# Optimization experiments

Hardware: AMD Instinct MI355X
Metric: run time of the kernel (lower is better)

The kernel has to match this reference:

```python
import jax, jax.numpy as jnp
import numpy as np

N_NODES = 10000
N_EDGES = 160000
N_TYPES = 128          # rows in SymbolicEmbeddingsVQ table
N_SYMBOLS = 64
PATTERN_LEN = 8
SYMBOL_DIM = 16
HIDDEN = PATTERN_LEN * SYMBOL_DIM  # mode='concat' -> 128
NUM_RADIAL = 6


def setup_inputs() -> dict:
    key = jax.random.key(0)
    ks = jax.random.split(key, 10)
    x = jax.random.randint(ks[0], (N_NODES,), 0, N_TYPES)
    rbf = jax.random.normal(ks[1], (N_EDGES, NUM_RADIAL), dtype=jnp.float32)
    i = jax.random.randint(ks[2], (N_EDGES,), 0, N_NODES)
    j = jax.random.randint(ks[3], (N_EDGES,), 0, N_NODES)
    # VQ symbolic embedding params: each of 128 types is a pattern of
    # PATTERN_LEN symbol ids; symbols are vectors from a codebook.
    code_idx = jax.random.randint(ks[4], (N_TYPES, PATTERN_LEN), 0, N_SYMBOLS)
    codebook = jax.random.normal(ks[5], (N_SYMBOLS, SYMBOL_DIM), dtype=jnp.float32)
    # Linear layers (PyTorch Linear default uniform init approximated by scaled normals)
    W_rbf = jax.random.normal(ks[6], (NUM_RADIAL, HIDDEN), dtype=jnp.float32) / np.sqrt(NUM_RADIAL)
    b_rbf = jnp.zeros((HIDDEN,), dtype=jnp.float32)
    W = jax.random.normal(ks[7], (3 * HIDDEN, HIDDEN), dtype=jnp.float32) / np.sqrt(3 * HIDDEN)
    b = jnp.zeros((HIDDEN,), dtype=jnp.float32)
    return {"x": x, "rbf": rbf, "i": i, "j": j, "code_idx": code_idx,
            "codebook": codebook, "W_rbf": W_rbf, "b_rbf": b_rbf, "W": W, "b": b}


def reference(x, rbf, i, j, code_idx, codebook, W_rbf, b_rbf, W, b):
    act = jax.nn.silu
    # Symbolic VQ embedding, mode='concat': table[t] = concat of PATTERN_LEN codebook vectors
    table = codebook[code_idx].reshape(N_TYPES, HIDDEN)   # [128, hidden]
    h = table[x]                                          # [N_nodes, hidden]
    r = act(rbf @ W_rbf + b_rbf)                          # [E, hidden]
    feat = jnp.concatenate([h[i], h[j], r], axis=-1)      # [E, 3*hidden]
    return act(feat @ W + b)                              # [E, hidden]
```

## Files before the change

kernel.cpp:

```cpp
#include <hip/hip_runtime.h>
#include <hip/hip_bf16.h>
#include <stdint.h>

typedef __attribute__((ext_vector_type(8))) short bf16x8;
typedef __attribute__((ext_vector_type(4))) float f32x4;

__device__ __forceinline__ float silu_f(float x) {
    return x / (1.0f + __expf(-x));
}

__device__ __forceinline__ unsigned short f2bf(float x) {
    union { float f; unsigned int u; } v; v.f = x;
    unsigned int r = v.u + 0x7fffu + ((v.u >> 16) & 1u);
    return (unsigned short)(r >> 16);
}
__device__ __forceinline__ float bf2f(unsigned short u) {
    union { unsigned int u; float f; } v; v.u = ((unsigned int)u) << 16;
    return v.f;
}

__device__ __forceinline__ void async16(void* l, const void* g) {
    auto lds3 = (__attribute__((address_space(3))) unsigned int*)(uintptr_t)l;
    auto g1   = (const __attribute__((address_space(1))) unsigned int*)(uintptr_t)g;
    __builtin_amdgcn_global_load_lds(g1, lds3, 16, 0, 0);
}

__global__ void prep_P(const int* __restrict__ code_idx,
                       const float* __restrict__ codebook,
                       const float* __restrict__ W,
                       const float* __restrict__ b,
                       unsigned short* __restrict__ P1,
                       unsigned short* __restrict__ P2,
                       unsigned short* __restrict__ Wt3)
{
    __shared__ float trow[128];
    const int t = blockIdx.x, tid = threadIdx.x;
    if (tid < 128) {
        int sym = code_idx[t * 8 + (tid >> 4)];
        trow[tid] = codebook[sym * 16 + (tid & 15)];
    } else {
        int k = tid - 128;
        Wt3[t * 128 + k] = f2bf(W[(256 + k) * 128 + t]);
    }
    __syncthreads();
    const int which = tid >> 7, o = tid & 127;
    const float* Wb = W + which * 16384;
    float acc = which ? 0.0f : b[o];
#pragma unroll 8
    for (int k = 0; k < 128; ++k)
        acc += trow[k] * Wb[k * 128 + o];
    (which ? P2 : P1)[t * 128 + o] = f2bf(acc);
}

__global__ __launch_bounds__(256, 2) void fused_main(
    const int* __restrict__ x,
    const float* __restrict__ rbf,
    const int* __restrict__ ei,
    const int* __restrict__ ej,
    const float* __restrict__ W_rbf,
    const float* __restrict__ b_rbf,
    const unsigned short* __restrict__ P1,
    const unsigned short* __restrict__ P2,
    const unsigned short* __restrict__ Wt3,
    float* __restrict__ out)
{
    __shared__ __align__(16) unsigned char lA[32768];
    __shared__ __align__(16) unsigned char lB[32768];

    const int tid  = threadIdx.x;
    const int lane = tid & 63;
    const int w    = tid >> 6;
    const int e0   = blockIdx.x * 128;

    {
        const int ri = lane >> 4;
        const int ch = lane & 15;
#pragma unroll
        for (int rr = 0; rr < 8; ++rr) {
            int g = w * 8 + rr;
            int o = g * 4 + ri;
            int j = ch ^ (o & 7);
            async16(lB + g * 1024, Wt3 + o * 128 + j * 8);
        }
    }

    {
        const int j16 = tid & 15;
        const int gg  = tid >> 4;
        const int cb  = j16 * 8;
        float wr[6][8];
#pragma unroll
        for (int q = 0; q < 6; ++q) {
            const float4* p = (const float4*)(W_rbf + q * 128 + cb);
            float4 a = p[0], c = p[1];
            wr[q][0]=a.x; wr[q][1]=a.y; wr[q][2]=a.z; wr[q][3]=a.w;
            wr[q][4]=c.x; wr[q][5]=c.y; wr[q][6]=c.z; wr[q][7]=c.w;
        }
        float br[8];
        {
            const float4* p = (const float4*)(b_rbf + cb);
            float4 a = p[0], c = p[1];
            br[0]=a.x; br[1]=a.y; br[2]=a.z; br[3]=a.w;
            br[4]=c.x; br[5]=c.y; br[6]=c.z; br[7]=c.w;
        }
#pragma unroll
        for (int i = 0; i < 8; ++i) {
            int m = gg * 8 + i;
            const float* rr = rbf + (size_t)(e0 + m) * 6;
            float f0=rr[0], f1=rr[1], f2=rr[2], f3=rr[3], f4=rr[4], f5=rr[5];
            bf16x8 pk;
#pragma unroll
            for (int c = 0; c < 8; ++c) {
                float acc = br[c] + f0*wr[0][c] + f1*wr[1][c] + f2*wr[2][c]
                                  + f3*wr[3][c] + f4*wr[4][c] + f5*wr[5][c];
                pk[c] = (short)f2bf(silu_f(acc));
            }
            int p = j16 ^ (m & 7);
            *(bf16x8*)(lA + m * 256 + p * 16) = pk;
        }
    }

    __syncthreads();

    f32x4 acc[4][4] = {};
    const int wm = (w >> 1) * 64, wn = (w & 1) * 64;
    const int quad = lane >> 4, l15 = lane & 15, l7 = lane & 7;
#pragma unroll
    for (int ks = 0; ks < 4; ++ks) {
        const int j = ks * 4 + quad;
        const int p = j ^ l7;
        bf16x8 af[4], bfv[4];
#pragma unroll
        for (int mi = 0; mi < 4; ++mi) {
            int m = wm + mi * 16 + l15;
            af[mi]  = *(const bf16x8*)(lA + m * 256 + p * 16);
            int o = wn + mi * 16 + l15;
            bfv[mi] = *(const bf16x8*)(lB + o * 256 + p * 16);
        }
#pragma unroll
        for (int mi = 0; mi < 4; ++mi)
#pragma unroll
            for (int ni = 0; ni < 4; ++ni)
                acc[mi][ni] = __builtin_amdgcn_mfma_f32_16x16x32_bf16(
                    af[mi], bfv[ni], acc[mi][ni], 0, 0, 0);
    }

#pragma unroll
    for (int mi = 0; mi < 4; ++mi) {
#pragma unroll
        for (int r = 0; r < 4; ++r) {
            int m = wm + mi * 16 + quad * 4 + r;
            int e = e0 + m;
            int ti = x[ei[e]], tj = x[ej[e]];
            const unsigned short* p1r = P1 + ti * 128;
            const unsigned short* p2r = P2 + tj * 128;
#pragma unroll
            for (int ni = 0; ni < 4; ++ni) {
                int o = wn + ni * 16 + l15;
                float v = acc[mi][ni][r] + bf2f(p1r[o]) + bf2f(p2r[o]);
                out[(size_t)e * 128 + o] = silu_f(v);
            }
        }
    }
}

extern "C" void kernel_launch(void* const* d_in, const int* in_sizes, int n_in,
                              void* d_out, int out_size, void* d_ws, size_t ws_size,
                              hipStream_t stream) {
    const int*   x        = (const int*)d_in[0];
    const float* rbf      = (const float*)d_in[1];
    const int*   ei       = (const int*)d_in[2];
    const int*   ej       = (const int*)d_in[3];
    const int*   code_idx = (const int*)d_in[4];
    const float* codebook = (const float*)d_in[5];
    const float* W_rbf    = (const float*)d_in[6];
    const float* b_rbf    = (const float*)d_in[7];
    const float* W        = (const float*)d_in[8];
    const float* b        = (const float*)d_in[9];
    float* out = (float*)d_out;

    const int nE = in_sizes[2];

    if (ws_size < 98304) return;
    unsigned short* P1  = (unsigned short*)d_ws;
    unsigned short* P2  = P1 + 16384;
    unsigned short* Wt3 = P2 + 16384;

    prep_P<<<128, 256, 0, stream>>>(code_idx, codebook, W, b, P1, P2, Wt3);
    fused_main<<<nE / 128, 256, 0, stream>>>(x, rbf, ei, ej, W_rbf, b_rbf,
                                             P1, P2, Wt3, out);
}
```

Baseline: 142.9 us.

## Halve edge tile, stage rbf via async LDS load, prefetch gather indices early

Halves the edges per block from 128 to 64, which shrinks LDS for the A tile and raises the occupancy hint to 3 blocks per SM. The rbf rows are now loaded into LDS with async global-to-LDS copies. The x[ei]/x[ej] index gathers and the P1/P2 row loads are issued before the MFMA loop, so their latency overlaps the rbf compute and the matmul. Silu now uses a hardware reciprocal instead of a division. In exchange, each block reloads the 32KB Wt3 tile for half as many edges, doubling that traffic, and the extra barrier adds sync cost.

```diff
diff --git a/kernel.cpp b/kernel.cpp
--- a/kernel.cpp
+++ b/kernel.cpp
@@ -6,7 +6,7 @@
 typedef __attribute__((ext_vector_type(4))) float f32x4;
 
 __device__ __forceinline__ float silu_f(float x) {
-    return x / (1.0f + __expf(-x));
+    return x * __builtin_amdgcn_rcpf(1.0f + __expf(-x));
 }
 
 __device__ __forceinline__ unsigned short f2bf(float x) {
@@ -52,7 +52,7 @@
     (which ? P2 : P1)[t * 128 + o] = f2bf(acc);
 }
 
-__global__ __launch_bounds__(256, 2) void fused_main(
+__global__ __launch_bounds__(256, 3) void fused_main(
     const int* __restrict__ x,
     const float* __restrict__ rbf,
     const int* __restrict__ ei,
@@ -64,17 +64,20 @@
     const unsigned short* __restrict__ Wt3,
     float* __restrict__ out)
 {
-    __shared__ __align__(16) unsigned char lA[32768];
     __shared__ __align__(16) unsigned char lB[32768];
+    __shared__ __align__(16) unsigned char lA[16384];
+    __shared__ __align__(16) unsigned char lR[1536];
 
     const int tid  = threadIdx.x;
     const int lane = tid & 63;
     const int w    = tid >> 6;
-    const int e0   = blockIdx.x * 128;
+    const int e0   = blockIdx.x * 64;
+
+    const int quad = lane >> 4, l15 = lane & 15;
+    const int wm = (w >> 1) * 32, wn = (w & 1) * 64;
 
     {
-        const int ri = lane >> 4;
-        const int ch = lane & 15;
+        const int ri = lane >> 4, ch = lane & 15;
 #pragma unroll
         for (int rr = 0; rr < 8; ++rr) {
             int g = w * 8 + rr;
@@ -83,62 +86,89 @@
             async16(lB + g * 1024, Wt3 + o * 128 + j * 8);
         }
     }
-
+    if (w == 0)
+        async16(lR, (const unsigned char*)rbf + (size_t)e0 * 24 + lane * 16);
+    else if (w == 1 && lane < 32)
+        async16(lR + 1024, (const unsigned char*)rbf + (size_t)e0 * 24 + 1024 + lane * 16);
+
+    int ti[8], tj[8];
+#pragma unroll
+    for (int mi = 0; mi < 2; ++mi)
+#pragma unroll
+        for (int r = 0; r < 4; ++r) {
+            int m = wm + mi * 16 + quad * 4 + r;
+            int e = e0 + m;
+            ti[mi * 4 + r] = x[ei[e]];
+            tj[mi * 4 + r] = x[ej[e]];
+        }
+
+    const int j16 = tid & 15, gg = tid >> 4, cb = j16 * 8;
+    float wr[6][8], br[8];
+#pragma unroll
+    for (int q = 0; q < 6; ++q) {
+        const float4* p = (const float4*)(W_rbf + q * 128 + cb);
+        float4 a = p[0], c = p[1];
+        wr[q][0]=a.x; wr[q][1]=a.y; wr[q][2]=a.z; wr[q][3]=a.w;
+        wr[q][4]=c.x; wr[q][5]=c.y; wr[q][6]=c.z; wr[q][7]=c.w;
+    }
     {
-        const int j16 = tid & 15;
-        const int gg  = tid >> 4;
-        const int cb  = j16 * 8;
-        float wr[6][8];
-#pragma unroll
-        for (int q = 0; q < 6; ++q) {
-            const float4* p = (const float4*)(W_rbf + q * 128 + cb);
-            float4 a = p[0], c = p[1];
-            wr[q][0]=a.x; wr[q][1]=a.y; wr[q][2]=a.z; wr[q][3]=a.w;
-            wr[q][4]=c.x; wr[q][5]=c.y; wr[q][6]=c.z; wr[q][7]=c.w;
-        }
-        float br[8];
-        {
-            const float4* p = (const float4*)(b_rbf + cb);
-            float4 a = p[0], c = p[1];
-            br[0]=a.x; br[1]=a.y; br[2]=a.z; br[3]=a.w;
-            br[4]=c.x; br[5]=c.y; br[6]=c.z; br[7]=c.w;
-        }
-#pragma unroll
-        for (int i = 0; i < 8; ++i) {
-            int m = gg * 8 + i;
-            const float* rr = rbf + (size_t)(e0 + m) * 6;
-            float f0=rr[0], f1=rr[1], f2=rr[2], f3=rr[3], f4=rr[4], f5=rr[5];
-            bf16x8 pk;
-#pragma unroll
-            for (int c = 0; c < 8; ++c) {
-                float acc = br[c] + f0*wr[0][c] + f1*wr[1][c] + f2*wr[2][c]
-                                  + f3*wr[3][c] + f4*wr[4][c] + f5*wr[5][c];
-                pk[c] = (short)f2bf(silu_f(acc));
+        const float4* p = (const float4*)(b_rbf + cb);
+        float4 a = p[0], c = p[1];
+        br[0]=a.x; br[1]=a.y; br[2]=a.z; br[3]=a.w;
+        br[4]=c.x; br[5]=c.y; br[6]=c.z; br[7]=c.w;
+    }
+
+    __syncthreads();
+
+#pragma unroll
+    for (int i = 0; i < 4; ++i) {
+        int m = gg * 4 + i;
+        const float* rr_ = (const float*)(lR + m * 24);
+        float f0 = rr_[0], f1 = rr_[1], f2 = rr_[2],
+              f3 = rr_[3], f4 = rr_[4], f5 = rr_[5];
+        bf16x8 pk;
+#pragma unroll
+        for (int c = 0; c < 8; ++c) {
+            float a = br[c] + f0*wr[0][c] + f1*wr[1][c] + f2*wr[2][c]
+                            + f3*wr[3][c] + f4*wr[4][c] + f5*wr[5][c];
+            pk[c] = (short)f2bf(silu_f(a));
+        }
+        int p = j16 ^ (m & 7);
+        *(bf16x8*)(lA + m * 256 + p * 16) = pk;
+    }
+
+    __syncthreads();
+
+    unsigned short q1[2][4][4], q2[2][4][4];
+#pragma unroll
+    for (int mi = 0; mi < 2; ++mi)
+#pragma unroll
+        for (int r = 0; r < 4; ++r) {
+            const unsigned short* p1r = P1 + ti[mi * 4 + r] * 128;
+            const unsigned short* p2r = P2 + tj[mi * 4 + r] * 128;
+#pragma unroll
+            for (int ni = 0; ni < 4; ++ni) {
+                int o = wn + ni * 16 + l15;
+                q1[mi][r][ni] = p1r[o];
+                q2[mi][r][ni] = p2r[o];
             }
-            int p = j16 ^ (m & 7);
-            *(bf16x8*)(lA + m * 256 + p * 16) = pk;
-        }
-    }
-
-    __syncthreads();
-
-    f32x4 acc[4][4] = {};
-    const int wm = (w >> 1) * 64, wn = (w & 1) * 64;
-    const int quad = lane >> 4, l15 = lane & 15, l7 = lane & 7;
+        }
+
+    f32x4 acc[2][4] = {};
+    const int l7 = l15 & 7;
 #pragma unroll
     for (int ks = 0; ks < 4; ++ks) {
         const int j = ks * 4 + quad;
         const int p = j ^ l7;
-        bf16x8 af[4], bfv[4];
-#pragma unroll
-        for (int mi = 0; mi < 4; ++mi) {
-            int m = wm + mi * 16 + l15;
-            af[mi]  = *(const bf16x8*)(lA + m * 256 + p * 16);
-            int o = wn + mi * 16 + l15;
-            bfv[mi] = *(const bf16x8*)(lB + o * 256 + p * 16);
-        }
-#pragma unroll
-        for (int mi = 0; mi < 4; ++mi)
+        bf16x8 af[2], bfv[4];
+#pragma unroll
+        for (int mi = 0; mi < 2; ++mi)
+            af[mi] = *(const bf16x8*)(lA + (wm + mi * 16 + l15) * 256 + p * 16);
+#pragma unroll
+        for (int ni = 0; ni < 4; ++ni)
+            bfv[ni] = *(const bf16x8*)(lB + (wn + ni * 16 + l15) * 256 + p * 16);
+#pragma unroll
+        for (int mi = 0; mi < 2; ++mi)
 #pragma unroll
             for (int ni = 0; ni < 4; ++ni)
                 acc[mi][ni] = __builtin_amdgcn_mfma_f32_16x16x32_bf16(
@@ -146,22 +176,18 @@
     }
 
 #pragma unroll
-    for (int mi = 0; mi < 4; ++mi) {
+    for (int mi = 0; mi < 2; ++mi)
 #pragma unroll
         for (int r = 0; r < 4; ++r) {
             int m = wm + mi * 16 + quad * 4 + r;
-            int e = e0 + m;
-            int ti = x[ei[e]], tj = x[ej[e]];
-            const unsigned short* p1r = P1 + ti * 128;
-            const unsigned short* p2r = P2 + tj * 128;
+            size_t e = e0 + m;
 #pragma unroll
             for (int ni = 0; ni < 4; ++ni) {
                 int o = wn + ni * 16 + l15;
-                float v = acc[mi][ni][r] + bf2f(p1r[o]) + bf2f(p2r[o]);
-                out[(size_t)e * 128 + o] = silu_f(v);
+                float v = acc[mi][ni][r] + bf2f(q1[mi][r][ni]) + bf2f(q2[mi][r][ni]);
+                out[e * 128 + o] = silu_f(v);
             }
         }
-    }
 }
 
 extern "C" void kernel_launch(void* const* d_in, const int* in_sizes, int n_in,
@@ -187,6 +213,6 @@
     unsigned short* Wt3 = P2 + 16384;
 
     prep_P<<<128, 256, 0, stream>>>(code_idx, codebook, W, b, P1, P2, Wt3);
-    fused_main<<<nE / 128, 256, 0, stream>>>(x, rbf, ei, ej, W_rbf, b_rbf,
-                                             P1, P2, Wt3, out);
-}
+    fused_main<<<nE / 64, 256, 0, stream>>>(x, rbf, ei, ej, W_rbf, b_rbf,
+                                            P1, P2, Wt3, out);
+}
```

New measurement: 132.9 us. 1.08x faster.
